# Kernel optimization log

Measured on AMD Instinct MI355X. Metric: run time of the kernel, lower is better.

## Reference

```python
import jax, jax.numpy as jnp
import numpy as np

# Module dims (match init_kwargs)
S = 8          # sequence_count
Q = 4          # queries_per_sequence
NS = 8         # ns_token_count
H = 256        # hidden_dim
N = S * Q      # number of independent query-generator heads
G = (S + NS) * H  # global_info_dim = 4096
EPS = 1e-5


def setup_inputs() -> dict:
    key = jax.random.key(0)
    ks = jax.random.split(key, 10)
    B = 256
    ns_tokens = jax.random.normal(ks[0], (B, NS, H), dtype=jnp.float32)
    sequence_pools = jax.random.normal(ks[1], (B, S, H), dtype=jnp.float32)
    # Stacked per-head parameters (head axis N first)
    ln_w = jnp.ones((N, G), dtype=jnp.float32)
    ln_b = jnp.zeros((N, G), dtype=jnp.float32)
    W1 = jax.random.normal(ks[2], (N, G, 2 * H), dtype=jnp.float32) / np.sqrt(G)
    b1 = jnp.zeros((N, 2 * H), dtype=jnp.float32)
    W2 = jax.random.normal(ks[3], (N, 2 * H, H), dtype=jnp.float32) / np.sqrt(2 * H)
    b2 = jnp.zeros((N, H), dtype=jnp.float32)
    query_embeddings = jax.random.normal(ks[4], (S, Q, H), dtype=jnp.float32) * 0.02
    return {
        "ns_tokens": ns_tokens,
        "sequence_pools": sequence_pools,
        "ln_w": ln_w,
        "ln_b": ln_b,
        "W1": W1,
        "b1": b1,
        "W2": W2,
        "b2": b2,
        "query_embeddings": query_embeddings,
    }


def reference(ns_tokens, sequence_pools, ln_w, ln_b, W1, b1, W2, b2, query_embeddings):
    B = ns_tokens.shape[0]
    # global_info: [B, G] = concat(flat ns_tokens, flat sequence_pools)
    gi = jnp.concatenate(
        [ns_tokens.reshape(B, -1), sequence_pools.reshape(B, -1)], axis=-1
    )
    # LayerNorm statistics are shared across heads (same input); only the
    # per-head affine (ln_w, ln_b) differs, so normalize once and fold the
    # affine into the first GEMM to avoid a [B, N, G] intermediate.
    mu = jnp.mean(gi, axis=-1, keepdims=True)
    var = jnp.mean(jnp.square(gi - mu), axis=-1, keepdims=True)
    xn = (gi - mu) * jax.lax.rsqrt(var + EPS)  # [B, G]
    # h[b,n,d] = sum_g xn[b,g] * ln_w[n,g] * W1[n,g,d] + ln_b[n,:] @ W1[n] + b1[n]
    h = jnp.einsum("bg,ng,ngd->bnd", xn, ln_w, W1)
    h = h + jnp.einsum("ng,ngd->nd", ln_b, W1) + b1  # [B, N, 2H]
    h = jax.nn.silu(h)
    # Dropout is inference-mode identity (module eval semantics).
    out = jnp.einsum("bnd,ndh->bnh", h, W2) + b2  # [B, N, H]
    out = out.reshape(B, S, Q, H)
    out = out + query_embeddings[None] + sequence_pools[:, :, None, :]
    return out
```

## Files before the change

### kernel.cpp

```cpp
#include <hip/hip_runtime.h>
#include <hip/hip_fp16.h>

typedef _Float16 h8v __attribute__((ext_vector_type(8)));
typedef __fp16   hf8 __attribute__((ext_vector_type(8)));
typedef float    f4v __attribute__((ext_vector_type(4)));
typedef unsigned int u32;

#define DEV __device__ __forceinline__

constexpr int NB    = 256;
constexpr int NHD   = 32;
constexpr int GG    = 4096;
constexpr int KHALF = 2048;
constexpr int D1    = 512;
constexpr int HD    = 256;

DEV int swz(int row, int c) {
    return row*32 + ((((c>>2) ^ (row & 7)) & 7) << 2) + (c & 3);
}
DEV u32 pk2(float a, float b) {
    auto r = __builtin_amdgcn_cvt_pkrtz(a, b);
    return __builtin_bit_cast(u32, r);
}
DEV f4v mfma16(h8v a, hf8 b, f4v c) {
    return __builtin_amdgcn_mfma_f32_16x16x32_f16(
        __builtin_bit_cast(hf8, a), b, c, 0, 0, 0);
}

__global__ __launch_bounds__(256) void k_prep(
        const float* __restrict__ ns, const float* __restrict__ pools,
        const float* __restrict__ lnw, const float* __restrict__ lnb,
        _Float16* __restrict__ xnh, _Float16* __restrict__ lnwh,
        _Float16* __restrict__ lnbh)
{
    const int t = threadIdx.x;
    const int bid = blockIdx.x;
    if (bid < NB) {
        f4v v[4];
        float s = 0.f, s2 = 0.f;
        #pragma unroll
        for (int p = 0; p < 4; ++p) {
            int i4 = t + 256*p;
            const float* src = (i4 < 512) ? (ns + (size_t)bid*2048 + i4*4)
                                          : (pools + (size_t)bid*2048 + (i4-512)*4);
            v[p] = *(const f4v*)src;
            #pragma unroll
            for (int j = 0; j < 4; ++j) { s += v[p][j]; s2 += v[p][j]*v[p][j]; }
        }
        #pragma unroll
        for (int o = 32; o > 0; o >>= 1) { s += __shfl_down(s, o); s2 += __shfl_down(s2, o); }
        __shared__ float red[8];
        if ((t & 63) == 0) { red[t>>6] = s; red[4 + (t>>6)] = s2; }
        __syncthreads();
        float ts   = red[0]+red[1]+red[2]+red[3];
        float ts2  = red[4]+red[5]+red[6]+red[7];
        float mu   = ts  * (1.f/4096.f);
        float var  = ts2 * (1.f/4096.f) - mu*mu;
        float rstd = rsqrtf(var + 1e-5f);
        #pragma unroll
        for (int p = 0; p < 4; ++p) {
            int i4 = t + 256*p;
            u32 w0 = pk2((v[p][0]-mu)*rstd, (v[p][1]-mu)*rstd);
            u32 w1 = pk2((v[p][2]-mu)*rstd, (v[p][3]-mu)*rstd);
            *(uint2*)(xnh + (size_t)bid*GG + i4*4) = make_uint2(w0, w1);
        }
    } else {
        const int base = (bid - NB)*2048 + t*8;
        f4v a0 = *(const f4v*)(lnw + base);
        f4v a1 = *(const f4v*)(lnw + base + 4);
        *(uint2*)(lnwh + base)     = make_uint2(pk2(a0[0],a0[1]), pk2(a0[2],a0[3]));
        *(uint2*)(lnwh + base + 4) = make_uint2(pk2(a1[0],a1[1]), pk2(a1[2],a1[3]));
        f4v c0 = *(const f4v*)(lnb + base);
        f4v c1 = *(const f4v*)(lnb + base + 4);
        *(uint2*)(lnbh + base)     = make_uint2(pk2(c0[0],c0[1]), pk2(c0[2],c0[3]));
        *(uint2*)(lnbh + base + 4) = make_uint2(pk2(c1[0],c1[1]), pk2(c1[2],c1[3]));
    }
}

__global__ __launch_bounds__(256, 2) void k_gemm1(
        const _Float16* __restrict__ xnh, const _Float16* __restrict__ lnwh,
        const _Float16* __restrict__ lnbh, const float* __restrict__ W1,
        float* __restrict__ hp)
{
    const int dt = blockIdx.x;
    const int n  = blockIdx.y;
    const int ks = blockIdx.z;
    const int t  = threadIdx.x;
    const int l  = t & 63;
    const int w  = t >> 6;

    __shared__ u32 lb[64*32];

    const float*    W1p = W1  + ((size_t)n*GG + (size_t)ks*KHALF)*D1 + dt*64;
    const _Float16* xb  = xnh + ks*KHALF;
    const _Float16* lwp = lnwh + (size_t)n*GG + ks*KHALF;
    const _Float16* lbp = lnbh + (size_t)n*GG + ks*KHALF;

    const int d0 = 4*(t & 15);
    const int g0 = 4*(t >> 4);
    int wp[4];
    #pragma unroll
    for (int i = 0; i < 4; ++i) wp[i] = swz(d0 + i, g0 >> 1);

    int rp[2][4];
    #pragma unroll
    for (int kc = 0; kc < 2; ++kc)
        #pragma unroll
        for (int ni = 0; ni < 4; ++ni) {
            int nr = ni*16 + (l & 15);
            int qq = kc*4 + (l >> 4);
            rp[kc][ni] = nr*32 + (((qq ^ (nr & 7)) & 7) << 2);
        }

    f4v st[4];
    #pragma unroll
    for (int p = 0; p < 4; ++p)
        st[p] = *(const f4v*)(W1p + (size_t)(g0 + p)*D1 + d0);

    f4v acc[4][4];
    #pragma unroll
    for (int mi = 0; mi < 4; ++mi)
        #pragma unroll
        for (int ni = 0; ni < 4; ++ni)
            #pragma unroll
            for (int r = 0; r < 4; ++r) acc[mi][ni][r] = 0.f;

    const int r0 = w*64;

    for (int kt = 0; kt < KHALF/64; ++kt) {
        __syncthreads();
        #pragma unroll
        for (int i = 0; i < 4; ++i) {
            u32 lo = pk2(st[0][i], st[1][i]);
            u32 hi = pk2(st[2][i], st[3][i]);
            *(uint2*)&lb[wp[i]] = make_uint2(lo, hi);
        }
        __syncthreads();
        if (kt + 1 < KHALF/64) {
            const float* src = W1p + (size_t)(kt + 1)*64*D1;
            #pragma unroll
            for (int p = 0; p < 4; ++p)
                st[p] = *(const f4v*)(src + (size_t)(g0 + p)*D1 + d0);
        }
        #pragma unroll
        for (int kc = 0; kc < 2; ++kc) {
            const int ko = kt*64 + kc*32 + 8*(l >> 4);
            h8v lw8 = *(const h8v*)(lwp + ko);
            h8v lb8 = *(const h8v*)(lbp + ko);
            h8v a[4];
            #pragma unroll
            for (int mi = 0; mi < 4; ++mi) {
                const _Float16* ap = xb + (size_t)(r0 + mi*16 + (l & 15))*GG + ko;
                h8v x = *(const h8v*)ap;
                a[mi] = x*lw8 + lb8;
            }
            #pragma unroll
            for (int ni = 0; ni < 4; ++ni) {
                hf8 bf = __builtin_bit_cast(hf8, *(const uint4*)&lb[rp[kc][ni]]);
                #pragma unroll
                for (int mi = 0; mi < 4; ++mi)
                    acc[mi][ni] = mfma16(a[mi], bf, acc[mi][ni]);
            }
        }
    }

    float* outp = hp + (size_t)ks*NB*NHD*D1;
    #pragma unroll
    for (int mi = 0; mi < 4; ++mi)
        #pragma unroll
        for (int ni = 0; ni < 4; ++ni)
            #pragma unroll
            for (int r = 0; r < 4; ++r) {
                int brow = r0 + mi*16 + (l >> 4)*4 + r;
                int dd   = dt*64 + ni*16 + (l & 15);
                outp[((size_t)brow*NHD + n)*D1 + dd] = acc[mi][ni][r];
            }
}

__global__ __launch_bounds__(256, 2) void k_gemm2(
        const float* __restrict__ hp, const float* __restrict__ b1,
        const float* __restrict__ W2, const float* __restrict__ b2,
        const float* __restrict__ qe, const float* __restrict__ pools,
        float* __restrict__ out)
{
    const int ht = blockIdx.x;
    const int bt = blockIdx.y;
    const int n  = blockIdx.z;
    const int t  = threadIdx.x;
    const int l  = t & 63;
    const int w  = t >> 6;
    const int wr = w >> 1, wc = w & 1;

    __shared__ u32 la[64*32];
    __shared__ u32 lbs[64*32];

    const size_t HPH = (size_t)NB*NHD*D1;
    const float* W2p = W2 + (size_t)n*D1*HD + ht*64;

    const int d0 = 4*(t & 15);
    const int g0 = 4*(t >> 4);
    const int ar = t >> 4;
    const int ak = 4*(t & 15);

    int wpB[4], wpA[4];
    #pragma unroll
    for (int i = 0; i < 4; ++i) wpB[i] = swz(d0 + i, g0 >> 1);
    #pragma unroll
    for (int p = 0; p < 4; ++p) wpA[p] = swz(ar + 16*p, ak >> 1);

    f4v acc[2][2];
    #pragma unroll
    for (int mi = 0; mi < 2; ++mi)
        #pragma unroll
        for (int ni = 0; ni < 2; ++ni)
            #pragma unroll
            for (int r = 0; r < 4; ++r) acc[mi][ni][r] = 0.f;

    for (int kt = 0; kt < D1/64; ++kt) {
        __syncthreads();
        #pragma unroll
        for (int p = 0; p < 4; ++p) {
            int r = ar + 16*p;
            size_t ro = ((size_t)(bt*64 + r)*NHD + n)*D1 + kt*64 + ak;
            f4v x0 = *(const f4v*)(hp + ro);
            f4v x1 = *(const f4v*)(hp + HPH + ro);
            f4v bb = *(const f4v*)(b1 + n*D1 + kt*64 + ak);
            float y[4];
            #pragma unroll
            for (int j = 0; j < 4; ++j) {
                float xv = x0[j] + x1[j] + bb[j];
                y[j] = xv / (1.f + __expf(-xv));
            }
            *(uint2*)&la[wpA[p]] = make_uint2(pk2(y[0], y[1]), pk2(y[2], y[3]));
        }
        f4v sw[4];
        #pragma unroll
        for (int p = 0; p < 4; ++p)
            sw[p] = *(const f4v*)(W2p + (size_t)(kt*64 + g0 + p)*HD + d0);
        #pragma unroll
        for (int i = 0; i < 4; ++i)
            *(uint2*)&lbs[wpB[i]] = make_uint2(pk2(sw[0][i], sw[1][i]), pk2(sw[2][i], sw[3][i]));
        __syncthreads();
        #pragma unroll
        for (int kc = 0; kc < 2; ++kc) {
            h8v a[2]; hf8 bf[2];
            #pragma unroll
            for (int mi = 0; mi < 2; ++mi) {
                int row = wr*32 + mi*16 + (l & 15);
                int qq  = kc*4 + (l >> 4);
                a[mi] = __builtin_bit_cast(h8v, *(const uint4*)&la[row*32 + (((qq ^ (row & 7)) & 7) << 2)]);
            }
            #pragma unroll
            for (int ni = 0; ni < 2; ++ni) {
                int col = wc*32 + ni*16 + (l & 15);
                int qq  = kc*4 + (l >> 4);
                bf[ni] = __builtin_bit_cast(hf8, *(const uint4*)&lbs[col*32 + (((qq ^ (col & 7)) & 7) << 2)]);
            }
            #pragma unroll
            for (int mi = 0; mi < 2; ++mi)
                #pragma unroll
                for (int ni = 0; ni < 2; ++ni)
                    acc[mi][ni] = mfma16(a[mi], bf[ni], acc[mi][ni]);
        }
    }

    const int s = n >> 2;
    #pragma unroll
    for (int mi = 0; mi < 2; ++mi)
        #pragma unroll
        for (int ni = 0; ni < 2; ++ni) {
            int hh = ht*64 + wc*32 + ni*16 + (l & 15);
            float add0 = b2[n*HD + hh] + qe[n*HD + hh];
            #pragma unroll
            for (int r = 0; r < 4; ++r) {
                int brow = bt*64 + wr*32 + mi*16 + (l >> 4)*4 + r;
                float v = acc[mi][ni][r] + add0 + pools[(size_t)brow*2048 + s*256 + hh];
                out[(size_t)brow*(NHD*HD) + n*HD + hh] = v;
            }
        }
}

extern "C" void kernel_launch(void* const* d_in, const int* in_sizes, int n_in,
                              void* d_out, int out_size, void* d_ws, size_t ws_size,
                              hipStream_t stream) {
    const float* ns   = (const float*)d_in[0];
    const float* pool = (const float*)d_in[1];
    const float* lnw  = (const float*)d_in[2];
    const float* lnb  = (const float*)d_in[3];
    const float* W1   = (const float*)d_in[4];
    const float* b1   = (const float*)d_in[5];
    const float* W2   = (const float*)d_in[6];
    const float* b2   = (const float*)d_in[7];
    const float* qe   = (const float*)d_in[8];
    float* out = (float*)d_out;

    char* ws = (char*)d_ws;
    _Float16* xnh  = (_Float16*)ws;
    _Float16* lnwh = (_Float16*)(ws + (2u << 20));
    _Float16* lnbh = (_Float16*)(ws + (2u << 20) + (256u << 10));
    float*    hp   = (float*)(ws + (4u << 20));

    hipLaunchKernelGGL(k_prep,  dim3(320),      dim3(256), 0, stream,
                       ns, pool, lnw, lnb, xnh, lnwh, lnbh);
    hipLaunchKernelGGL(k_gemm1, dim3(8, 32, 2), dim3(256), 0, stream,
                       xnh, lnwh, lnbh, W1, hp);
    hipLaunchKernelGGL(k_gemm2, dim3(4, 4, 32), dim3(256), 0, stream,
                       hp, b1, W2, b2, qe, pool, out);
}
```

Measured before the change: 451.5 us.

## Fold LayerNorm affine into W1 staging and restructure second GEMM tiling

The LayerNorm scale is now applied to W1 while it is staged into shared memory, and the LayerNorm bias contribution (lnb·W1) is accumulated separately as a per-head bias vector. This replaces the per-element affine on activations inside the MFMA loop. W2 is converted to fp16 in the prep kernel. GEMM1 output is written in a fragment-native blocked layout so stores are contiguous, and GEMM2 reads that layout directly with a new 32x128 tile and a flattened grid. The trade-offs are an extra fp16 W2 pass, more workspace, and rounding W1·lnw to fp16.

```diff
diff --git a/kernel.cpp b/kernel.cpp
--- a/kernel.cpp
+++ b/kernel.cpp
@@ -8,12 +8,10 @@
 
 #define DEV __device__ __forceinline__
 
-constexpr int NB    = 256;
-constexpr int NHD   = 32;
-constexpr int GG    = 4096;
-constexpr int KHALF = 2048;
-constexpr int D1    = 512;
-constexpr int HD    = 256;
+constexpr int NB  = 256;
+constexpr int GG  = 4096;
+constexpr int D1  = 512;
+constexpr int HD  = 256;
 
 DEV int swz(int row, int c) {
     return row*32 + ((((c>>2) ^ (row & 7)) & 7) << 2) + (c & 3);
@@ -22,6 +20,10 @@
     auto r = __builtin_amdgcn_cvt_pkrtz(a, b);
     return __builtin_bit_cast(u32, r);
 }
+DEV u32 packh(_Float16 lo, _Float16 hi) {
+    return (u32)__builtin_bit_cast(unsigned short, lo)
+         | ((u32)__builtin_bit_cast(unsigned short, hi) << 16);
+}
 DEV f4v mfma16(h8v a, hf8 b, f4v c) {
     return __builtin_amdgcn_mfma_f32_16x16x32_f16(
         __builtin_bit_cast(hf8, a), b, c, 0, 0, 0);
@@ -29,9 +31,8 @@
 
 __global__ __launch_bounds__(256) void k_prep(
         const float* __restrict__ ns, const float* __restrict__ pools,
-        const float* __restrict__ lnw, const float* __restrict__ lnb,
-        _Float16* __restrict__ xnh, _Float16* __restrict__ lnwh,
-        _Float16* __restrict__ lnbh)
+        const float* __restrict__ W2,
+        _Float16* __restrict__ xnh, _Float16* __restrict__ w2h)
 {
     const int t = threadIdx.x;
     const int bid = blockIdx.x;
@@ -65,22 +66,19 @@
             *(uint2*)(xnh + (size_t)bid*GG + i4*4) = make_uint2(w0, w1);
         }
     } else {
-        const int base = (bid - NB)*2048 + t*8;
-        f4v a0 = *(const f4v*)(lnw + base);
-        f4v a1 = *(const f4v*)(lnw + base + 4);
-        *(uint2*)(lnwh + base)     = make_uint2(pk2(a0[0],a0[1]), pk2(a0[2],a0[3]));
-        *(uint2*)(lnwh + base + 4) = make_uint2(pk2(a1[0],a1[1]), pk2(a1[2],a1[3]));
-        f4v c0 = *(const f4v*)(lnb + base);
-        f4v c1 = *(const f4v*)(lnb + base + 4);
-        *(uint2*)(lnbh + base)     = make_uint2(pk2(c0[0],c0[1]), pk2(c0[2],c0[3]));
-        *(uint2*)(lnbh + base + 4) = make_uint2(pk2(c1[0],c1[1]), pk2(c1[2],c1[3]));
+        const size_t base = (size_t)(bid - NB)*2048 + t*8;
+        f4v a0 = *(const f4v*)(W2 + base);
+        f4v a1 = *(const f4v*)(W2 + base + 4);
+        uint4 o; o.x = pk2(a0[0],a0[1]); o.y = pk2(a0[2],a0[3]);
+                 o.z = pk2(a1[0],a1[1]); o.w = pk2(a1[2],a1[3]);
+        *(uint4*)(w2h + base) = o;
     }
 }
 
 __global__ __launch_bounds__(256, 2) void k_gemm1(
-        const _Float16* __restrict__ xnh, const _Float16* __restrict__ lnwh,
-        const _Float16* __restrict__ lnbh, const float* __restrict__ W1,
-        float* __restrict__ hp)
+        const _Float16* __restrict__ xnh, const float* __restrict__ lnw,
+        const float* __restrict__ lnb, const float* __restrict__ W1,
+        float* __restrict__ hp, float* __restrict__ bias_p)
 {
     const int dt = blockIdx.x;
     const int n  = blockIdx.y;
@@ -91,10 +89,10 @@
 
     __shared__ u32 lb[64*32];
 
-    const float*    W1p = W1  + ((size_t)n*GG + (size_t)ks*KHALF)*D1 + dt*64;
-    const _Float16* xb  = xnh + ks*KHALF;
-    const _Float16* lwp = lnwh + (size_t)n*GG + ks*KHALF;
-    const _Float16* lbp = lnbh + (size_t)n*GG + ks*KHALF;
+    const float* W1p = W1  + ((size_t)n*GG + (size_t)ks*2048)*D1 + dt*64;
+    const float* lwp = lnw + n*GG + ks*2048;
+    const float* lbp = lnb + n*GG + ks*2048;
+    const _Float16* xb = xnh + ks*2048;
 
     const int d0 = 4*(t & 15);
     const int g0 = 4*(t >> 4);
@@ -108,14 +106,21 @@
         #pragma unroll
         for (int ni = 0; ni < 4; ++ni) {
             int nr = ni*16 + (l & 15);
-            int qq = kc*4 + (l >> 4);
-            rp[kc][ni] = nr*32 + (((qq ^ (nr & 7)) & 7) << 2);
-        }
-
-    f4v st[4];
+            rp[kc][ni] = nr*32 + ((((kc*4 + (l >> 4)) ^ (nr & 7)) & 7) << 2);
+        }
+
+    const int r0 = w*64;
+    const _Float16* xrow[4];
+    #pragma unroll
+    for (int mi = 0; mi < 4; ++mi)
+        xrow[mi] = xb + (size_t)(r0 + mi*16 + (l & 15))*GG + 8*(l >> 4);
+
+    f4v st[4], lnwv, lnbv;
     #pragma unroll
     for (int p = 0; p < 4; ++p)
         st[p] = *(const f4v*)(W1p + (size_t)(g0 + p)*D1 + d0);
+    lnwv = *(const f4v*)(lwp + g0);
+    lnbv = *(const f4v*)(lbp + g0);
 
     f4v acc[4][4];
     #pragma unroll
@@ -124,89 +129,114 @@
         for (int ni = 0; ni < 4; ++ni)
             #pragma unroll
             for (int r = 0; r < 4; ++r) acc[mi][ni][r] = 0.f;
-
-    const int r0 = w*64;
-
-    for (int kt = 0; kt < KHALF/64; ++kt) {
-        __syncthreads();
+    f4v bacc; bacc[0]=bacc[1]=bacc[2]=bacc[3]=0.f;
+
+    for (int kt = 0; kt < 32; ++kt) {
+        __syncthreads();
+        f4v sc[4];
+        #pragma unroll
+        for (int p = 0; p < 4; ++p) {
+            bacc += lnbv[p] * st[p];
+            sc[p] = st[p] * lnwv[p];
+        }
         #pragma unroll
         for (int i = 0; i < 4; ++i) {
-            u32 lo = pk2(st[0][i], st[1][i]);
-            u32 hi = pk2(st[2][i], st[3][i]);
+            u32 lo = pk2(sc[0][i], sc[1][i]);
+            u32 hi = pk2(sc[2][i], sc[3][i]);
             *(uint2*)&lb[wp[i]] = make_uint2(lo, hi);
         }
         __syncthreads();
-        if (kt + 1 < KHALF/64) {
+        if (kt + 1 < 32) {
             const float* src = W1p + (size_t)(kt + 1)*64*D1;
             #pragma unroll
             for (int p = 0; p < 4; ++p)
                 st[p] = *(const f4v*)(src + (size_t)(g0 + p)*D1 + d0);
-        }
-        #pragma unroll
-        for (int kc = 0; kc < 2; ++kc) {
-            const int ko = kt*64 + kc*32 + 8*(l >> 4);
-            h8v lw8 = *(const h8v*)(lwp + ko);
-            h8v lb8 = *(const h8v*)(lbp + ko);
-            h8v a[4];
-            #pragma unroll
-            for (int mi = 0; mi < 4; ++mi) {
-                const _Float16* ap = xb + (size_t)(r0 + mi*16 + (l & 15))*GG + ko;
-                h8v x = *(const h8v*)ap;
-                a[mi] = x*lw8 + lb8;
-            }
+            lnwv = *(const f4v*)(lwp + (kt+1)*64 + g0);
+            lnbv = *(const f4v*)(lbp + (kt+1)*64 + g0);
+        }
+        h8v xa[2][4];
+        #pragma unroll
+        for (int kc = 0; kc < 2; ++kc)
+            #pragma unroll
+            for (int mi = 0; mi < 4; ++mi)
+                xa[kc][mi] = *(const h8v*)(xrow[mi] + kt*64 + kc*32);
+        #pragma unroll
+        for (int kc = 0; kc < 2; ++kc)
             #pragma unroll
             for (int ni = 0; ni < 4; ++ni) {
                 hf8 bf = __builtin_bit_cast(hf8, *(const uint4*)&lb[rp[kc][ni]]);
                 #pragma unroll
                 for (int mi = 0; mi < 4; ++mi)
-                    acc[mi][ni] = mfma16(a[mi], bf, acc[mi][ni]);
+                    acc[mi][ni] = mfma16(xa[kc][mi], bf, acc[mi][ni]);
             }
-        }
-    }
-
-    float* outp = hp + (size_t)ks*NB*NHD*D1;
+    }
+
+    __syncthreads();
+    float* fl = (float*)lb;
+    *(f4v*)(fl + 4*t) = bacc;
+    __syncthreads();
+    if (t < 64) {
+        float s = 0.f;
+        int c = t >> 2, i = t & 3;
+        #pragma unroll
+        for (int j = 0; j < 16; ++j) s += fl[(16*j + c)*4 + i];
+        bias_p[(ks*32 + n)*D1 + dt*64 + t] = s;
+    }
+
+    float* outp = hp + ((size_t)(ks*32 + n)*8 + dt)*16384;
     #pragma unroll
     for (int mi = 0; mi < 4; ++mi)
         #pragma unroll
         for (int ni = 0; ni < 4; ++ni)
             #pragma unroll
-            for (int r = 0; r < 4; ++r) {
-                int brow = r0 + mi*16 + (l >> 4)*4 + r;
-                int dd   = dt*64 + ni*16 + (l & 15);
-                outp[((size_t)brow*NHD + n)*D1 + dd] = acc[mi][ni][r];
-            }
+            for (int r = 0; r < 4; ++r)
+                outp[(((w*4 + mi)*4 + ni)*4 + r)*64 + l] = acc[mi][ni][r];
 }
 
 __global__ __launch_bounds__(256, 2) void k_gemm2(
-        const float* __restrict__ hp, const float* __restrict__ b1,
-        const float* __restrict__ W2, const float* __restrict__ b2,
-        const float* __restrict__ qe, const float* __restrict__ pools,
-        float* __restrict__ out)
+        const float* __restrict__ hp, const float* __restrict__ bias_p,
+        const float* __restrict__ b1, const _Float16* __restrict__ w2h,
+        const float* __restrict__ b2, const float* __restrict__ qe,
+        const float* __restrict__ pools, float* __restrict__ out)
 {
-    const int ht = blockIdx.x;
+    const int n  = blockIdx.x >> 1;
+    const int ht = blockIdx.x & 1;
     const int bt = blockIdx.y;
-    const int n  = blockIdx.z;
     const int t  = threadIdx.x;
     const int l  = t & 63;
-    const int w  = t >> 6;
-    const int wr = w >> 1, wc = w & 1;
-
-    __shared__ u32 la[64*32];
-    __shared__ u32 lbs[64*32];
-
-    const size_t HPH = (size_t)NB*NHD*D1;
-    const float* W2p = W2 + (size_t)n*D1*HD + ht*64;
-
-    const int d0 = 4*(t & 15);
-    const int g0 = 4*(t >> 4);
-    const int ar = t >> 4;
-    const int ak = 4*(t & 15);
-
-    int wpB[4], wpA[4];
-    #pragma unroll
-    for (int i = 0; i < 4; ++i) wpB[i] = swz(d0 + i, g0 >> 1);
-    #pragma unroll
-    for (int p = 0; p < 4; ++p) wpA[p] = swz(ar + 16*p, ak >> 1);
+    const int wc = t >> 6;
+
+    __shared__ u32 la[32*32];
+    __shared__ u32 lbs[128*32];
+
+    const int row32 = t >> 3, koff = (t & 7)*8;
+    const int brow  = bt*32 + row32;
+    const int Fo = (((brow>>6)*4 + ((brow>>4)&3))*4)*256 + (brow&3)*64 + ((brow>>2)&3)*16
+                 + ((koff>>4))*256 + (koff & 15);
+    const float* hp0 = hp + (size_t)n*8*16384 + Fo;
+    const float* hp1 = hp0 + (size_t)32*8*16384;
+    const float* bpp0 = bias_p + n*D1 + koff;
+    const float* bpp1 = bpp0 + 32*D1;
+    const float* b1p  = b1 + n*D1 + koff;
+    const int wpa = row32*32 + (((t & 7) ^ (row32 & 7)) << 2);
+
+    const int g0 = 4*(t >> 4), d0 = 8*(t & 15);
+    const _Float16* w2p = w2h + (size_t)n*D1*HD + ht*128 + d0;
+
+    int rpa[2][2], rpb[2][2];
+    #pragma unroll
+    for (int kc = 0; kc < 2; ++kc) {
+        #pragma unroll
+        for (int mi = 0; mi < 2; ++mi) {
+            int row = mi*16 + (l & 15);
+            rpa[kc][mi] = row*32 + ((((kc*4 + (l >> 4)) ^ (row & 7)) & 7) << 2);
+        }
+        #pragma unroll
+        for (int ni = 0; ni < 2; ++ni) {
+            int col = wc*32 + ni*16 + (l & 15);
+            rpb[kc][ni] = col*32 + ((((kc*4 + (l >> 4)) ^ (col & 7)) & 7) << 2);
+        }
+    }
 
     f4v acc[2][2];
     #pragma unroll
@@ -216,68 +246,73 @@
             #pragma unroll
             for (int r = 0; r < 4; ++r) acc[mi][ni][r] = 0.f;
 
-    for (int kt = 0; kt < D1/64; ++kt) {
-        __syncthreads();
-        #pragma unroll
-        for (int p = 0; p < 4; ++p) {
-            int r = ar + 16*p;
-            size_t ro = ((size_t)(bt*64 + r)*NHD + n)*D1 + kt*64 + ak;
-            f4v x0 = *(const f4v*)(hp + ro);
-            f4v x1 = *(const f4v*)(hp + HPH + ro);
-            f4v bb = *(const f4v*)(b1 + n*D1 + kt*64 + ak);
-            float y[4];
-            #pragma unroll
-            for (int j = 0; j < 4; ++j) {
-                float xv = x0[j] + x1[j] + bb[j];
-                y[j] = xv / (1.f + __expf(-xv));
-            }
-            *(uint2*)&la[wpA[p]] = make_uint2(pk2(y[0], y[1]), pk2(y[2], y[3]));
-        }
-        f4v sw[4];
+    for (int kt = 0; kt < 8; ++kt) {
+        f4v a00 = *(const f4v*)(hp0 + kt*16384);
+        f4v a01 = *(const f4v*)(hp0 + kt*16384 + 4);
+        f4v a10 = *(const f4v*)(hp1 + kt*16384);
+        f4v a11 = *(const f4v*)(hp1 + kt*16384 + 4);
+        f4v p0a = *(const f4v*)(bpp0 + kt*64), p0b = *(const f4v*)(bpp0 + kt*64 + 4);
+        f4v p1a = *(const f4v*)(bpp1 + kt*64), p1b = *(const f4v*)(bpp1 + kt*64 + 4);
+        f4v b1a = *(const f4v*)(b1p + kt*64),  b1b = *(const f4v*)(b1p + kt*64 + 4);
+        h8v wv[4];
         #pragma unroll
         for (int p = 0; p < 4; ++p)
-            sw[p] = *(const f4v*)(W2p + (size_t)(kt*64 + g0 + p)*HD + d0);
-        #pragma unroll
-        for (int i = 0; i < 4; ++i)
-            *(uint2*)&lbs[wpB[i]] = make_uint2(pk2(sw[0][i], sw[1][i]), pk2(sw[2][i], sw[3][i]));
+            wv[p] = *(const h8v*)(w2p + (size_t)(kt*64 + g0 + p)*HD);
+
+        __syncthreads();
+        f4v x0 = a00 + a10 + p0a + p1a + b1a;
+        f4v x1 = a01 + a11 + p0b + p1b + b1b;
+        float y[8];
+        #pragma unroll
+        for (int j = 0; j < 4; ++j) {
+            y[j]   = __fdividef(x0[j], 1.f + __expf(-x0[j]));
+            y[4+j] = __fdividef(x1[j], 1.f + __expf(-x1[j]));
+        }
+        uint4 pa;
+        pa.x = pk2(y[0],y[1]); pa.y = pk2(y[2],y[3]);
+        pa.z = pk2(y[4],y[5]); pa.w = pk2(y[6],y[7]);
+        *(uint4*)&la[wpa] = pa;
+        #pragma unroll
+        for (int j0 = 0; j0 < 8; ++j0) {
+            int j = (j0 + (t & 7)) & 7;
+            int col = d0 + j;
+            u32 lo = packh(wv[0][j], wv[1][j]);
+            u32 hi = packh(wv[2][j], wv[3][j]);
+            int off = col*32 + ((((t >> 5) ^ (col & 7)) & 7) << 2) + ((g0 >> 1) & 3);
+            *(uint2*)&lbs[off] = make_uint2(lo, hi);
+        }
         __syncthreads();
         #pragma unroll
         for (int kc = 0; kc < 2; ++kc) {
-            h8v a[2]; hf8 bf[2];
-            #pragma unroll
-            for (int mi = 0; mi < 2; ++mi) {
-                int row = wr*32 + mi*16 + (l & 15);
-                int qq  = kc*4 + (l >> 4);
-                a[mi] = __builtin_bit_cast(h8v, *(const uint4*)&la[row*32 + (((qq ^ (row & 7)) & 7) << 2)]);
-            }
-            #pragma unroll
-            for (int ni = 0; ni < 2; ++ni) {
-                int col = wc*32 + ni*16 + (l & 15);
-                int qq  = kc*4 + (l >> 4);
-                bf[ni] = __builtin_bit_cast(hf8, *(const uint4*)&lbs[col*32 + (((qq ^ (col & 7)) & 7) << 2)]);
-            }
+            h8v af[2]; hf8 bf[2];
+            #pragma unroll
+            for (int mi = 0; mi < 2; ++mi)
+                af[mi] = __builtin_bit_cast(h8v, *(const uint4*)&la[rpa[kc][mi]]);
+            #pragma unroll
+            for (int ni = 0; ni < 2; ++ni)
+                bf[ni] = __builtin_bit_cast(hf8, *(const uint4*)&lbs[rpb[kc][ni]]);
             #pragma unroll
             for (int mi = 0; mi < 2; ++mi)
                 #pragma unroll
                 for (int ni = 0; ni < 2; ++ni)
-                    acc[mi][ni] = mfma16(a[mi], bf[ni], acc[mi][ni]);
+                    acc[mi][ni] = mfma16(af[mi], bf[ni], acc[mi][ni]);
         }
     }
 
     const int s = n >> 2;
     #pragma unroll
-    for (int mi = 0; mi < 2; ++mi)
-        #pragma unroll
-        for (int ni = 0; ni < 2; ++ni) {
-            int hh = ht*64 + wc*32 + ni*16 + (l & 15);
-            float add0 = b2[n*HD + hh] + qe[n*HD + hh];
+    for (int ni = 0; ni < 2; ++ni) {
+        int hh = ht*128 + wc*32 + ni*16 + (l & 15);
+        float add0 = b2[n*HD + hh] + qe[n*HD + hh];
+        #pragma unroll
+        for (int mi = 0; mi < 2; ++mi)
             #pragma unroll
             for (int r = 0; r < 4; ++r) {
-                int brow = bt*64 + wr*32 + mi*16 + (l >> 4)*4 + r;
-                float v = acc[mi][ni][r] + add0 + pools[(size_t)brow*2048 + s*256 + hh];
-                out[(size_t)brow*(NHD*HD) + n*HD + hh] = v;
+                int br = bt*32 + mi*16 + (l >> 4)*4 + r;
+                out[((size_t)br*32 + n)*HD + hh] =
+                    acc[mi][ni][r] + add0 + pools[(size_t)br*2048 + s*HD + hh];
             }
-        }
+    }
 }
 
 extern "C" void kernel_launch(void* const* d_in, const int* in_sizes, int n_in,
@@ -295,15 +330,15 @@
     float* out = (float*)d_out;
 
     char* ws = (char*)d_ws;
-    _Float16* xnh  = (_Float16*)ws;
-    _Float16* lnwh = (_Float16*)(ws + (2u << 20));
-    _Float16* lnbh = (_Float16*)(ws + (2u << 20) + (256u << 10));
-    float*    hp   = (float*)(ws + (4u << 20));
-
-    hipLaunchKernelGGL(k_prep,  dim3(320),      dim3(256), 0, stream,
-                       ns, pool, lnw, lnb, xnh, lnwh, lnbh);
-    hipLaunchKernelGGL(k_gemm1, dim3(8, 32, 2), dim3(256), 0, stream,
-                       xnh, lnwh, lnbh, W1, hp);
-    hipLaunchKernelGGL(k_gemm2, dim3(4, 4, 32), dim3(256), 0, stream,
-                       hp, b1, W2, b2, qe, pool, out);
-}
+    _Float16* xnh    = (_Float16*)ws;
+    _Float16* w2h    = (_Float16*)(ws + (2u  << 20));
+    float*    bias_p = (float*)   (ws + (10u << 20));
+    float*    hp     = (float*)   (ws + (16u << 20));
+
+    hipLaunchKernelGGL(k_prep,  dim3(NB + 2048), dim3(256), 0, stream,
+                       ns, pool, W2, xnh, w2h);
+    hipLaunchKernelGGL(k_gemm1, dim3(8, 32, 2),  dim3(256), 0, stream,
+                       xnh, lnw, lnb, W1, hp, bias_p);
+    hipLaunchKernelGGL(k_gemm2, dim3(64, 8),     dim3(256), 0, stream,
+                       hp, bias_p, b1, w2h, b2, qe, pool, out);
+}
```

Measured after the change: 446.5 us. About the same (-1.1%).
